# Kernel optimization log

Measured on AMD Instinct MI355X. Metric: run time of the kernel, lower is better.

Reference implementation:

```python
import jax, jax.numpy as jnp
import numpy as np
from jax import lax

# minLSTM activation g(x) = x + 0.5 if x >= 0 else sigmoid(x)  (mingru repo functional.g)

def g_act(x):
    return jnp.where(x >= 0, x + 0.5, jax.nn.sigmoid(x))


def conv2d_seq(x5, w, b):
    # x5: (B,S,Cin,H,W), w: (Cout,Cin,3,3), stride 1, pad 1 -> (B,S,Cout,H,W)
    B, S = x5.shape[:2]
    xf = x5.reshape((B * S,) + x5.shape[2:])
    y = lax.conv_general_dilated(xf, w, window_strides=(1, 1),
                                 padding=[(1, 1), (1, 1)],
                                 dimension_numbers=("NCHW", "OIHW", "NCHW"))
    y = y + b[None, :, None, None]
    return y.reshape((B, S) + y.shape[1:])


def minlstm_layer(inp, w, b):
    # inp: (B,S,Cin,H,W) -> out h: (B,S,Cout,H,W)
    gates = conv2d_seq(inp, w, b)                     # (B,S,4C,H,W)
    i_g, f_g, o_g, cand = jnp.split(gates, 4, axis=2)  # each (B,S,C,H,W)
    it = jax.nn.sigmoid(i_g)
    ft = jax.nn.sigmoid(f_g)
    denom = it + ft
    fp = ft / denom                                   # normalized forget gate
    ig = (it / denom) * g_act(cand)                   # normalized input * candidate
    B, S, C, H, W = fp.shape
    # zero-init cell state passes through g: g(0) = 0.5 (init_hidden_state)
    c0 = jnp.full((B, C, H, W), 0.5, dtype=inp.dtype)

    def step(c, xs):
        fpt, igt = xs
        c_new = fpt * c + igt
        return c_new, c_new

    xs = (jnp.moveaxis(fp, 1, 0), jnp.moveaxis(ig, 1, 0))  # (S,B,C,H,W)
    _, cs = lax.scan(step, c0, xs)
    cs = jnp.moveaxis(cs, 0, 1)                       # (B,S,C,H,W)
    h = jax.nn.sigmoid(o_g) * cs                      # output gate
    return h


def setup_inputs() -> dict:
    key = jax.random.key(0)
    ks = jax.random.split(key, 5)
    x = jax.random.normal(ks[0], (4, 16, 32, 32, 32), dtype=jnp.float32)
    w0 = jax.random.normal(ks[1], (256, 32, 3, 3), dtype=jnp.float32) * 0.05
    b0 = jax.random.normal(ks[2], (256,), dtype=jnp.float32) * 0.05
    w1 = jax.random.normal(ks[3], (256, 64, 3, 3), dtype=jnp.float32) * 0.05
    b1 = jax.random.normal(ks[4], (256,), dtype=jnp.float32) * 0.05
    return {"x": x, "w0": w0, "b0": b0, "w1": w1, "b1": b1}


def reference(x, w0, b0, w1, b1):
    out = minlstm_layer(x, w0, b0)
    out = minlstm_layer(out, w1, b1)
    return out  # (B,S,64,H,W) — last layer outputs
```

## Files before the change

### kernel.cpp

```cpp
#include <hip/hip_runtime.h>


typedef __bf16 bf16x8 __attribute__((ext_vector_type(8)));
typedef __bf16 bf16x4 __attribute__((ext_vector_type(4)));
typedef __bf16 bf16x2 __attribute__((ext_vector_type(2)));
typedef float f32x4 __attribute__((ext_vector_type(4)));

#define N_IMG 64
#define HP 34
#define COUT 256

__device__ __forceinline__ float sigf(float x) { return 1.0f / (1.0f + __expf(-x)); }

__device__ __forceinline__ void gload16(void* lds, const void* g) {
  __builtin_amdgcn_global_load_lds(
      (const __attribute__((address_space(1))) void*)g,
      (__attribute__((address_space(3))) void*)lds, 16, 0, 0);
}

__global__ __launch_bounds__(256) void pack_x_k(const float* __restrict__ x,
                                                __bf16* __restrict__ xT) {
  __shared__ float ls[32][33];
  const int n = blockIdx.x >> 5;
  const int h = blockIdx.x & 31;
  const int t = threadIdx.x;
  {
    const int w = t & 31, g4 = t >> 5;
    const float* src = x + (((size_t)n * 32) << 10) + (h << 5);
#pragma unroll
    for (int j = 0; j < 4; ++j) {
      int ci = g4 * 4 + j;
      ls[ci][w] = src[((size_t)ci << 10) + w];
    }
  }
  __syncthreads();
  {
    const int ci = t & 31, w4 = t >> 5;
    __bf16* dst = xT + ((size_t)(n * HP + h + 1) * HP + 1) * 32 + ci;
#pragma unroll
    for (int j = 0; j < 4; ++j) {
      int w = w4 * 4 + j;
      dst[w * 32] = (__bf16)ls[ci][w];
    }
  }
}

template <int CIN>
__global__ __launch_bounds__(256) void pack_w_k(const float* __restrict__ w,
                                                __bf16* __restrict__ wT) {
  int g = blockIdx.x * 256 + threadIdx.x;
  if (g >= 256 * 9 * CIN) return;
  int co = g / (9 * CIN);
  int r = g - co * 9 * CIN;
  int khkw = r / CIN;
  int ci = r - khkw * CIN;
  wT[g] = (__bf16)w[(size_t)(co * CIN + ci) * 9 + khkw];
}

template <int CIN, bool LAYER1>
__global__ __launch_bounds__(256, 2) void conv_gemm_k(
    const __bf16* __restrict__ xT,
    const __bf16* __restrict__ wT,
    const float* __restrict__ bias,
    __bf16* __restrict__ gates) {
  constexpr int NKK = CIN / 32;
  constexpr int CHUNKS = CIN / 8;
  constexpr int PLANE = 204;
  __shared__ bf16x8 lsA[CHUNKS * PLANE];
  __shared__ bf16x8 lsB[2][CHUNKS * 128];

  const int tid = threadIdx.x;
  const int lane = tid & 63;
  const int wid = tid >> 6;
  const int wr = wid >> 1, wc = wid & 1;
  const int g = lane >> 4;
  const int li = lane & 15;

  const int bx = blockIdx.x;
  const int by = blockIdx.y;
  const int n = bx >> 3;
  const int h0 = (bx & 7) << 2;
  const int co0 = by << 7;

  f32x4 acc[4][4] = {};
  const size_t wrow = (size_t)9 * CIN;

  for (int gi = tid; gi < CHUNKS * PLANE; gi += 256) {
    const int ch = gi & (CHUNKS - 1);
    const int pos = gi / CHUNKS;
    const int r = pos / 34;
    const int w = pos - r * 34;
    lsA[ch * PLANE + pos] = *reinterpret_cast<const bf16x8*>(
        xT + ((size_t)(n * HP + h0 + r) * HP + w) * CIN + ch * 8);
  }

  int posm[4];
#pragma unroll
  for (int mi = 0; mi < 4; ++mi) {
    const int m = wr * 64 + mi * 16 + li;
    posm[mi] = (m >> 5) * 34 + (m & 31);
  }

  auto stageB = [&](int buf, int t) {
#pragma unroll
    for (int c = wid; c < 2 * CHUNKS; c += 4) {
      const int chunk = c >> 1;
      const int row = ((c & 1) << 6) + lane;
      gload16((void*)(&lsB[buf][c * 64]),
              (const void*)(wT + (size_t)(co0 + row) * wrow + t * CIN + chunk * 8));
    }
  };

  stageB(0, 0);
  __syncthreads();
  int cur = 0;
#pragma unroll
  for (int t = 0; t < 9; ++t) {
    const int kh = t / 3;
    const int kw = t - kh * 3;
    const int tapoff = kh * 34 + kw;
    if (t < 8) stageB(cur ^ 1, t + 1);
#pragma unroll
    for (int kk = 0; kk < NKK; ++kk) {
      const int ca = kk * 4 + g;
      bf16x8 af[4], wf[4];
#pragma unroll
      for (int mi = 0; mi < 4; ++mi)
        af[mi] = lsA[ca * PLANE + posm[mi] + tapoff];
#pragma unroll
      for (int ni = 0; ni < 4; ++ni)
        wf[ni] = lsB[cur][ca * 128 + wc * 64 + ni * 16 + li];
#pragma unroll
      for (int mi = 0; mi < 4; ++mi)
#pragma unroll
        for (int ni = 0; ni < 4; ++ni) {
          if constexpr (!LAYER1)
            acc[mi][ni] = __builtin_amdgcn_mfma_f32_16x16x32_bf16(
                af[mi], wf[ni], acc[mi][ni], 0, 0, 0);
          else
            acc[mi][ni] = __builtin_amdgcn_mfma_f32_16x16x32_bf16(
                wf[ni], af[mi], acc[mi][ni], 0, 0, 0);
        }
    }
    __syncthreads();
    cur ^= 1;
  }

#pragma unroll
  for (int mi = 0; mi < 4; ++mi)
#pragma unroll
    for (int ni = 0; ni < 4; ++ni)
#pragma unroll
      for (int r = 0; r < 4; ++r) {
        if constexpr (!LAYER1) {
          const int m_loc = wr * 64 + mi * 16 + (g << 2) + r;
          const int co = co0 + wc * 64 + ni * 16 + li;
          const size_t m = (size_t)bx * 128 + m_loc;
          gates[m * 256 + co] = (__bf16)(acc[mi][ni][r] + bias[co]);
        } else {
          const int co = co0 + wc * 64 + ni * 16 + (g << 2) + r;
          const int m_loc = wr * 64 + mi * 16 + li;
          const int m = bx * 128 + m_loc;
          const int nimg = m >> 10, p = m & 1023;
          gates[((size_t)nimg * 256 + co) * 1024 + p] =
              (__bf16)(acc[mi][ni][r] + bias[co]);
        }
      }
}

__global__ __launch_bounds__(256) void scan0_k(const __bf16* __restrict__ gates,
                                               __bf16* __restrict__ h0T) {
  const int g = blockIdx.x * 256 + threadIdx.x;
  const int c = (g & 15) * 4;
  const int p = (g >> 4) & 1023;
  const int b = g >> 14;
  const int h = p >> 5, w = p & 31;
  float cst[4] = {0.5f, 0.5f, 0.5f, 0.5f};
#pragma unroll 4
  for (int s = 0; s < 16; ++s) {
    const size_t base = ((size_t)((b * 16 + s) * 1024 + p)) * 256 + c;
    const bf16x4* gp = reinterpret_cast<const bf16x4*>(gates + base);
    const bf16x4 ig4 = gp[0], fg4 = gp[16], og4 = gp[32], cd4 = gp[48];
    bf16x4 hv4;
#pragma unroll
    for (int j = 0; j < 4; ++j) {
      const float it = sigf((float)ig4[j]), ft = sigf((float)fg4[j]);
      const float inv = 1.0f / (it + ft);
      const float cd_ = (float)cd4[j];
      const float gc = (cd_ >= 0.0f) ? (cd_ + 0.5f) : sigf(cd_);
      cst[j] = (ft * inv) * cst[j] + (it * inv) * gc;
      hv4[j] = (__bf16)(sigf((float)og4[j]) * cst[j]);
    }
    *reinterpret_cast<bf16x4*>(
        h0T + ((size_t)((b * 16 + s) * HP + h + 1) * HP + (w + 1)) * 64 + c) = hv4;
  }
}

__global__ __launch_bounds__(256) void scan1_k(const __bf16* __restrict__ gates,
                                               float* __restrict__ out) {
  const int g = blockIdx.x * 256 + threadIdx.x;
  const int p0 = (g & 255) * 4;
  const int c = (g >> 8) & 63;
  const int b = g >> 14;
  float cst[4] = {0.5f, 0.5f, 0.5f, 0.5f};
#pragma unroll 2
  for (int s = 0; s < 16; ++s) {
    const size_t base = ((size_t)(b * 16 + s) * 256 + c) * 1024 + p0;
    const bf16x4 ig4 = *reinterpret_cast<const bf16x4*>(gates + base);
    const bf16x4 fg4 = *reinterpret_cast<const bf16x4*>(gates + base + 64 * 1024);
    const bf16x4 og4 = *reinterpret_cast<const bf16x4*>(gates + base + 128 * 1024);
    const bf16x4 cd4 = *reinterpret_cast<const bf16x4*>(gates + base + 192 * 1024);
    f32x4 hv;
#pragma unroll
    for (int j = 0; j < 4; ++j) {
      const float it = sigf((float)ig4[j]), ft = sigf((float)fg4[j]);
      const float inv = 1.0f / (it + ft);
      const float cd_ = (float)cd4[j];
      const float gc = (cd_ >= 0.0f) ? (cd_ + 0.5f) : sigf(cd_);
      cst[j] = (ft * inv) * cst[j] + (it * inv) * gc;
      hv[j] = sigf((float)og4[j]) * cst[j];
    }
    *reinterpret_cast<f32x4*>(
        out + ((size_t)((b * 16 + s) * 64 + c)) * 1024 + p0) = hv;
  }
}

extern "C" void kernel_launch(void* const* d_in, const int* in_sizes, int n_in,
                              void* d_out, int out_size, void* d_ws,
                              size_t ws_size, hipStream_t stream) {
  const float* x = (const float*)d_in[0];
  const float* w0 = (const float*)d_in[1];
  const float* b0 = (const float*)d_in[2];
  const float* w1 = (const float*)d_in[3];
  const float* b1 = (const float*)d_in[4];
  float* out = (float*)d_out;

  char* ws = (char*)d_ws;
  const size_t XT_BYTES = (size_t)N_IMG * HP * HP * 32 * 2;
  const size_t H0_BYTES = (size_t)N_IMG * HP * HP * 64 * 2;
  const size_t W0T_BYTES = (size_t)256 * 9 * 32 * 2;
  const size_t W1T_BYTES = (size_t)256 * 9 * 64 * 2;
  __bf16* xT = (__bf16*)ws;
  __bf16* h0T = (__bf16*)(ws + XT_BYTES);
  __bf16* w0T = (__bf16*)(ws + XT_BYTES + H0_BYTES);
  __bf16* w1T = (__bf16*)(ws + XT_BYTES + H0_BYTES + W0T_BYTES);
  __bf16* gates = (__bf16*)(ws + XT_BYTES + H0_BYTES + W0T_BYTES + W1T_BYTES);
  (void)ws_size; (void)n_in; (void)in_sizes; (void)out_size;

  hipMemsetAsync(xT, 0, XT_BYTES, stream);
  hipMemsetAsync(h0T, 0, H0_BYTES, stream);

  pack_x_k<<<N_IMG * 32, 256, 0, stream>>>(x, xT);
  pack_w_k<32><<<(256 * 9 * 32 + 255) / 256, 256, 0, stream>>>(w0, w0T);
  pack_w_k<64><<<(256 * 9 * 64 + 255) / 256, 256, 0, stream>>>(w1, w1T);

  conv_gemm_k<32, false><<<dim3(512, 2), 256, 0, stream>>>(xT, w0T, b0, gates);
  scan0_k<<<256, 256, 0, stream>>>(gates, h0T);
  conv_gemm_k<64, true><<<dim3(512, 2), 256, 0, stream>>>(h0T, w1T, b1, gates);
  scan1_k<<<256, 256, 0, stream>>>(gates, out);
}
```

Measured before the change: 165.7 us.

## Load conv weights directly into registers with triple buffering, dropping LDS staging

Repacks the weights into a chunk-major layout with output channels contiguous, so each lane can read its MFMA B fragments straight from global memory into registers. Prefetch runs two taps ahead using a 3-deep register buffer. This removes the LDS weight buffer and the per-tap __syncthreads barriers. The cost is much higher register pressure (3*NKK*4 bf16x8 per thread, 96 VGPRs for CIN=64) under launch bounds of 2 blocks per SM, which risks spills or lower occupancy, and global load latency is now exposed directly to the MFMA loop.

```diff
diff --git a/kernel.cpp b/kernel.cpp
--- a/kernel.cpp
+++ b/kernel.cpp
@@ -3,7 +3,6 @@
 
 typedef __bf16 bf16x8 __attribute__((ext_vector_type(8)));
 typedef __bf16 bf16x4 __attribute__((ext_vector_type(4)));
-typedef __bf16 bf16x2 __attribute__((ext_vector_type(2)));
 typedef float f32x4 __attribute__((ext_vector_type(4)));
 
 #define N_IMG 64
@@ -11,12 +10,6 @@
 #define COUT 256
 
 __device__ __forceinline__ float sigf(float x) { return 1.0f / (1.0f + __expf(-x)); }
-
-__device__ __forceinline__ void gload16(void* lds, const void* g) {
-  __builtin_amdgcn_global_load_lds(
-      (const __attribute__((address_space(1))) void*)g,
-      (__attribute__((address_space(3))) void*)lds, 16, 0, 0);
-}
 
 __global__ __launch_bounds__(256) void pack_x_k(const float* __restrict__ x,
                                                 __bf16* __restrict__ xT) {
@@ -47,27 +40,29 @@
 
 template <int CIN>
 __global__ __launch_bounds__(256) void pack_w_k(const float* __restrict__ w,
-                                                __bf16* __restrict__ wT) {
+                                                __bf16* __restrict__ wT3) {
+  constexpr int CHUNKS = CIN / 8;
   int g = blockIdx.x * 256 + threadIdx.x;
   if (g >= 256 * 9 * CIN) return;
-  int co = g / (9 * CIN);
-  int r = g - co * 9 * CIN;
-  int khkw = r / CIN;
-  int ci = r - khkw * CIN;
-  wT[g] = (__bf16)w[(size_t)(co * CIN + ci) * 9 + khkw];
+  const int j = g & 7;
+  const int co = (g >> 3) & 255;
+  const int r = g >> 11;
+  const int ca = r % CHUNKS;
+  const int t = r / CHUNKS;
+  const int ci = ca * 8 + j;
+  wT3[g] = (__bf16)w[(size_t)(co * CIN + ci) * 9 + t];
 }
 
 template <int CIN, bool LAYER1>
 __global__ __launch_bounds__(256, 2) void conv_gemm_k(
     const __bf16* __restrict__ xT,
-    const __bf16* __restrict__ wT,
+    const __bf16* __restrict__ wT3,
     const float* __restrict__ bias,
     __bf16* __restrict__ gates) {
   constexpr int NKK = CIN / 32;
   constexpr int CHUNKS = CIN / 8;
   constexpr int PLANE = 204;
   __shared__ bf16x8 lsA[CHUNKS * PLANE];
-  __shared__ bf16x8 lsB[2][CHUNKS * 128];
 
   const int tid = threadIdx.x;
   const int lane = tid & 63;
@@ -83,7 +78,6 @@
   const int co0 = by << 7;
 
   f32x4 acc[4][4] = {};
-  const size_t wrow = (size_t)9 * CIN;
 
   for (int gi = tid; gi < CHUNKS * PLANE; gi += 256) {
     const int ch = gi & (CHUNKS - 1);
@@ -101,49 +95,49 @@
     posm[mi] = (m >> 5) * 34 + (m & 31);
   }
 
-  auto stageB = [&](int buf, int t) {
-#pragma unroll
-    for (int c = wid; c < 2 * CHUNKS; c += 4) {
-      const int chunk = c >> 1;
-      const int row = ((c & 1) << 6) + lane;
-      gload16((void*)(&lsB[buf][c * 64]),
-              (const void*)(wT + (size_t)(co0 + row) * wrow + t * CIN + chunk * 8));
-    }
+  const bf16x8* wp = reinterpret_cast<const bf16x8*>(wT3);
+  const int cobase = co0 + wc * 64 + li;
+
+  bf16x8 wreg[3][NKK][4];
+  auto loadW = [&](int buf, int t) {
+#pragma unroll
+    for (int kk = 0; kk < NKK; ++kk)
+#pragma unroll
+      for (int ni = 0; ni < 4; ++ni)
+        wreg[buf][kk][ni] =
+            wp[(size_t)(t * CHUNKS + kk * 4 + g) * 256 + cobase + ni * 16];
   };
 
-  stageB(0, 0);
+  loadW(0, 0);
+  loadW(1, 1);
   __syncthreads();
-  int cur = 0;
+
 #pragma unroll
   for (int t = 0; t < 9; ++t) {
+    if (t < 7) loadW((t + 2) % 3, t + 2);
     const int kh = t / 3;
     const int kw = t - kh * 3;
     const int tapoff = kh * 34 + kw;
-    if (t < 8) stageB(cur ^ 1, t + 1);
+    const int buf = t % 3;
 #pragma unroll
     for (int kk = 0; kk < NKK; ++kk) {
       const int ca = kk * 4 + g;
-      bf16x8 af[4], wf[4];
+      bf16x8 af[4];
 #pragma unroll
       for (int mi = 0; mi < 4; ++mi)
         af[mi] = lsA[ca * PLANE + posm[mi] + tapoff];
-#pragma unroll
-      for (int ni = 0; ni < 4; ++ni)
-        wf[ni] = lsB[cur][ca * 128 + wc * 64 + ni * 16 + li];
 #pragma unroll
       for (int mi = 0; mi < 4; ++mi)
 #pragma unroll
         for (int ni = 0; ni < 4; ++ni) {
           if constexpr (!LAYER1)
             acc[mi][ni] = __builtin_amdgcn_mfma_f32_16x16x32_bf16(
-                af[mi], wf[ni], acc[mi][ni], 0, 0, 0);
+                af[mi], wreg[buf][kk][ni], acc[mi][ni], 0, 0, 0);
           else
             acc[mi][ni] = __builtin_amdgcn_mfma_f32_16x16x32_bf16(
-                wf[ni], af[mi], acc[mi][ni], 0, 0, 0);
+                wreg[buf][kk][ni], af[mi], acc[mi][ni], 0, 0, 0);
         }
     }
-    __syncthreads();
-    cur ^= 1;
   }
 
 #pragma unroll
```

Result: no change. 165.0 us (-0.4%).
